# Kernel tuning notes

Hardware: AMD Instinct MI355X
Metric: run time of the kernel (lower is better)

Reference implementation:

```python
import jax, jax.numpy as jnp
import numpy as np

B, CN, DEG, IN_F, OUT_F, K = 32, 1024, 2, 128, 128, 10
NODES = [1, 16, 128, 1024]


def setup_inputs() -> dict:
    key = jax.random.key(0)
    ks = jax.random.split(key, 16)
    d = {}
    for i, n in enumerate(NODES):
        d[f"tree{i}"] = jax.random.normal(ks[i], (B, n, IN_F), dtype=jnp.float32)
    for i in range(4):
        d[f"Uw{i}"] = jax.random.normal(ks[4 + i], (IN_F, OUT_F), dtype=jnp.float32) * 0.05
        d[f"Ub{i}"] = jnp.zeros((OUT_F,), dtype=jnp.float32)
    d["W_up"] = jax.random.normal(ks[8], (CN, IN_F, DEG * IN_F), dtype=jnp.float32) * 0.05
    d["Fw0"] = jax.random.normal(ks[9], (IN_F, K * IN_F), dtype=jnp.float32) * 0.05
    d["Fb0"] = jnp.zeros((K * IN_F,), dtype=jnp.float32)
    d["Fw1"] = jax.random.normal(ks[10], (K * IN_F, OUT_F), dtype=jnp.float32) * 0.05
    d["Fb1"] = jnp.zeros((OUT_F,), dtype=jnp.float32)
    d["b_bias"] = jax.random.normal(ks[11], (1, DEG * CN, OUT_F), dtype=jnp.float32) * 0.05
    return d


def reference(tree0, tree1, tree2, tree3,
              Uw0, Ub0, Uw1, Ub1, Uw2, Ub2, Uw3, Ub3,
              W_up, Fw0, Fb0, Fw1, Fb1, b_bias):
    tree = [tree0, tree1, tree2, tree3]
    Uw = [Uw0, Uw1, Uw2, Uw3]
    Ub = [Ub0, Ub1, Ub2, Ub3]
    curr_node = W_up.shape[0]
    in_feat = W_up.shape[1]
    degree = W_up.shape[2] // in_feat

    # Ancestor info: project each depth, then tile each ancestor node's
    # projected vector to cover its descendants at the current level.
    anc = jnp.zeros((tree[0].shape[0], curr_node, Uw0.shape[1]), dtype=tree0.dtype)
    for t, w, b in zip(tree, Uw, Ub):
        Q = t @ w + b                       # [B, anc_node, out_feat]
        rep = curr_node // t.shape[1]
        anc = anc + jnp.repeat(Q, rep, axis=1)  # == tf.tile([1,1,rep]) + reshape

    # Per-node unique-weight upsample: [B,n,1,in] @ [n,in,deg*in]
    nl = jnp.einsum('bni,nio->bno', tree[-1], W_up)            # [B, CN, deg*in]
    nl = nl.reshape(nl.shape[0], curr_node * degree, in_feat)   # [B, CN*deg, in]
    nl = (nl @ Fw0 + Fb0) @ Fw1 + Fb1                           # Dense chain
    nl = nl + jnp.repeat(anc, degree, axis=1)                   # broadcast ancestors
    nl = nl + b_bias
    return jnp.where(nl >= 0, nl, 0.2 * nl)                     # LeakyReLU(0.2)
```

## Files before the change

kernel.cpp:

```cpp
#include <hip/hip_runtime.h>
#include <stdint.h>


using short8   = __attribute__((ext_vector_type(8))) short;
using floatx16 = __attribute__((ext_vector_type(16))) float;

__device__ __forceinline__ unsigned short f2bf(float f) {
    unsigned int u = __builtin_bit_cast(unsigned int, f);
    return (unsigned short)((u + 0x8000u) >> 16);
}

#define FB_OFF  524288
#define FF_OFF  524416
#define UW_OFF  532608

__global__ __launch_bounds__(256) void ffused_p1(
    const float* __restrict__ Fw0, const float* __restrict__ Fb0,
    const float* __restrict__ Fw1, float* __restrict__ P)
{
    const int kc = blockIdx.x;
    const int i  = blockIdx.y;
    const int j  = threadIdx.x & 127;
    const int il = threadIdx.x >> 7;
    const int k0 = kc * 160 + il * 80;
    const float* __restrict__ src = (i < 128) ? (Fw0 + (size_t)i * 1280) : Fb0;
    float acc = 0.f;
    #pragma unroll 8
    for (int kk = 0; kk < 80; ++kk)
        acc += src[k0 + kk] * Fw1[(size_t)(k0 + kk) * 128 + j];
    P[(size_t)(kc * 2 + il) * 16512 + i * 128 + j] = acc;
}

__global__ __launch_bounds__(256) void prep2(
    const float* __restrict__ P, const float* __restrict__ Fb1,
    const float* __restrict__ Uw0, const float* __restrict__ Uw1,
    const float* __restrict__ Uw2, const float* __restrict__ Uw3,
    unsigned short* __restrict__ FfusedBF, float* __restrict__ Fbias,
    unsigned short* __restrict__ UwBF)
{
    if (blockIdx.x < 65) {
        const int idx = blockIdx.x * 256 + threadIdx.x;
        if (idx >= 16512) return;
        const int i = idx >> 7, j = idx & 127;
        float s = 0.f;
        #pragma unroll
        for (int p = 0; p < 16; ++p) s += P[(size_t)p * 16512 + idx];
        if (i < 128) FfusedBF[(((i >> 3) * 128) + j) * 8 + (i & 7)] = f2bf(s);
        else         Fbias[j] = s + Fb1[j];
    } else {
        const int bx  = blockIdx.x - 65;
        const int mat = bx >> 4;
        const int kg  = bx & 15;
        const float* __restrict__ Uw = (mat == 0) ? Uw0 : (mat == 1) ? Uw1
                                     : (mat == 2) ? Uw2 : Uw3;
        const int col = threadIdx.x & 127;
        const int kh  = threadIdx.x >> 7;
        #pragma unroll
        for (int q = 0; q < 4; ++q) {
            const int kk = kh * 4 + q;
            const float v = Uw[(size_t)(kg * 8 + kk) * 128 + col];
            UwBF[(((size_t)(mat * 16 + kg) * 128) + col) * 8 + kk] = f2bf(v);
        }
    }
}

__global__ __launch_bounds__(256, 2) void tree_main(
    const float* __restrict__ t0, const float* __restrict__ t1,
    const float* __restrict__ t2, const float* __restrict__ t3,
    const float* __restrict__ Ub0, const float* __restrict__ Ub1,
    const float* __restrict__ Ub2, const float* __restrict__ Ub3,
    const float* __restrict__ Wup, const float* __restrict__ bbias,
    const unsigned short* __restrict__ FfusedBF,
    const unsigned short* __restrict__ UwBF,
    const float* __restrict__ Fbias,
    float* __restrict__ out)
{
    const int n    = blockIdx.x;
    const int tid  = threadIdx.x;
    const int w    = tid >> 6;
    const int lane = tid & 63;
    const int l31  = lane & 31;
    const int half = lane >> 5;
    const int colq = w * 32 + l31;
    const int i2   = n >> 3;

    __shared__ __align__(16) unsigned char smem_raw[64 * 33 * 8 * 2];
    unsigned short* Alds = (unsigned short*)smem_raw;
    unsigned short* Ulds = (unsigned short*)smem_raw;

    const float* __restrict__ Wbase =
        Wup + (size_t)n * 32768 + (half * 8) * 256 + w * 64 + l31;
    float Wa0[8], Wa1[8], Wb0[8], Wb1[8], Wc0[8], Wc1[8], Wd0[8], Wd1[8];
#define LOADW(P0, P1, WT) \
    { const float* __restrict__ wp = Wbase + (WT) * 16 * 256; \
      _Pragma("unroll") \
      for (int jj = 0; jj < 8; ++jj) { P0[jj] = wp[jj * 256]; P1[jj] = wp[32 + jj * 256]; } }
    LOADW(Wa0, Wa1, 0) LOADW(Wb0, Wb1, 1) LOADW(Wc0, Wc1, 2) LOADW(Wd0, Wd1, 3)

    #pragma unroll
    for (int mi = 0; mi < 4; ++mi) {
        const float* __restrict__ base = (mi == 0) ? t0 : (mi == 1) ? t1
                                       : (mi == 2) ? t2 : t3;
        #pragma unroll
        for (int i = 0; i < 4; ++i) {
            const int idx = i * 256 + tid;
            const int b   = idx >> 5;
            const int q   = idx & 31;
            int row;
            if      (mi == 0) row = b;
            else if (mi == 1) row = b * 16 + (i2 >> 3);
            else if (mi == 2) row = b * 128 + i2;
            else              row = b * 1024 + n;
            const float4 v = *reinterpret_cast<const float4*>(
                base + (size_t)row * 128 + q * 4);
            ushort4 u;
            u.x = f2bf(v.x); u.y = f2bf(v.y); u.z = f2bf(v.z); u.w = f2bf(v.w);
            *reinterpret_cast<ushort4*>(
                &Alds[((mi * 16 + (q >> 1)) * 33 + b) * 8 + (q & 1) * 4]) = u;
        }
    }
    __syncthreads();

    floatx16 qacc, accT0, accT1;
    #pragma unroll
    for (int r = 0; r < 16; ++r) { qacc[r] = 0.f; accT0[r] = 0.f; accT1[r] = 0.f; }

    #pragma unroll
    for (int ks = 0; ks < 24; ++ks) {
        const int kg = 2 * ks + half;
        const short8 a  = *reinterpret_cast<const short8*>(&Alds[(kg * 33 + l31) * 8]);
        const short8 bf = *reinterpret_cast<const short8*>(
            &UwBF[((size_t)kg * 128 + colq) * 8]);
        qacc = __builtin_amdgcn_mfma_f32_32x32x16_bf16(a, bf, qacc, 0, 0, 0);
    }

#define WBODY(P0, P1, WT) \
    { const int kg = 48 + 2 * (WT) + half; \
      const short8 a  = *reinterpret_cast<const short8*>(&Alds[(kg * 33 + l31) * 8]); \
      const short8 bf = *reinterpret_cast<const short8*>( \
          &UwBF[((size_t)kg * 128 + colq) * 8]); \
      qacc = __builtin_amdgcn_mfma_f32_32x32x16_bf16(a, bf, qacc, 0, 0, 0); \
      short8 a0, a1; \
      _Pragma("unroll") \
      for (int jj = 0; jj < 8; ++jj) { \
          a0[jj] = (short)f2bf(P0[jj]); a1[jj] = (short)f2bf(P1[jj]); } \
      accT0 = __builtin_amdgcn_mfma_f32_32x32x16_bf16(a0, a, accT0, 0, 0, 0); \
      accT1 = __builtin_amdgcn_mfma_f32_32x32x16_bf16(a1, a, accT1, 0, 0, 0); }

    WBODY(Wa0, Wa1, 0) LOADW(Wa0, Wa1, 4)
    WBODY(Wb0, Wb1, 1) LOADW(Wb0, Wb1, 5)
    WBODY(Wc0, Wc1, 2) LOADW(Wc0, Wc1, 6)
    WBODY(Wd0, Wd1, 3) LOADW(Wd0, Wd1, 7)
    WBODY(Wa0, Wa1, 4)
    WBODY(Wb0, Wb1, 5)
    WBODY(Wc0, Wc1, 6)
    WBODY(Wd0, Wd1, 7)

    __syncthreads();

    #pragma unroll
    for (int tt = 0; tt < 2; ++tt) {
        const floatx16 Av = tt ? accT1 : accT0;
        #pragma unroll
        for (int r = 0; r < 16; ++r) {
            const int cm = w * 64 + tt * 32 + ((r & 3) + 8 * (r >> 2) + 4 * half);
            const int d  = cm >> 7;
            const int cp = cm & 127;
            Ulds[(((cp >> 3) * 65) + d * 32 + l31) * 8 + (cp & 7)] = f2bf(Av[r]);
        }
    }
    __syncthreads();

    const float ubsum = Ub0[colq] + Ub1[colq] + Ub2[colq] + Ub3[colq] + Fbias[colq];
    const float bb0 = bbias[(size_t)(2 * n + 0) * 128 + colq];
    const float bb1 = bbias[(size_t)(2 * n + 1) * 128 + colq];

    floatx16 o0, o1;
    #pragma unroll
    for (int r = 0; r < 16; ++r) { o0[r] = 0.f; o1[r] = 0.f; }
    #pragma unroll
    for (int ks = 0; ks < 8; ++ks) {
        const int kg2 = 2 * ks + half;
        const short8 a0 = *reinterpret_cast<const short8*>(&Ulds[(kg2 * 65 + l31) * 8]);
        const short8 a1 = *reinterpret_cast<const short8*>(&Ulds[(kg2 * 65 + 32 + l31) * 8]);
        const short8 bf = *reinterpret_cast<const short8*>(
            &FfusedBF[(((size_t)kg2 * 128) + colq) * 8]);
        o0 = __builtin_amdgcn_mfma_f32_32x32x16_bf16(a0, bf, o0, 0, 0, 0);
        o1 = __builtin_amdgcn_mfma_f32_32x32x16_bf16(a1, bf, o1, 0, 0, 0);
    }

    #pragma unroll
    for (int r = 0; r < 16; ++r) {
        const int brow = (r & 3) + 8 * (r >> 2) + 4 * half;
        const float addc = qacc[r] + ubsum;
        float v0 = o0[r] + addc + bb0;
        float v1 = o1[r] + addc + bb1;
        v0 = (v0 >= 0.f) ? v0 : 0.2f * v0;
        v1 = (v1 >= 0.f) ? v1 : 0.2f * v1;
        const size_t idx0 = ((size_t)brow * 2048 + 2 * n) * 128 + colq;
        out[idx0]       = v0;
        out[idx0 + 128] = v1;
    }
}

extern "C" void kernel_launch(void* const* d_in, const int* in_sizes, int n_in,
                              void* d_out, int out_size, void* d_ws, size_t ws_size,
                              hipStream_t stream) {
    const float* t0  = (const float*)d_in[0];
    const float* t1  = (const float*)d_in[1];
    const float* t2  = (const float*)d_in[2];
    const float* t3  = (const float*)d_in[3];
    const float* Uw0 = (const float*)d_in[4];
    const float* Ub0 = (const float*)d_in[5];
    const float* Uw1 = (const float*)d_in[6];
    const float* Ub1 = (const float*)d_in[7];
    const float* Uw2 = (const float*)d_in[8];
    const float* Ub2 = (const float*)d_in[9];
    const float* Uw3 = (const float*)d_in[10];
    const float* Ub3 = (const float*)d_in[11];
    const float* Wup = (const float*)d_in[12];
    const float* Fw0 = (const float*)d_in[13];
    const float* Fb0 = (const float*)d_in[14];
    const float* Fw1 = (const float*)d_in[15];
    const float* Fb1 = (const float*)d_in[16];
    const float* bb  = (const float*)d_in[17];

    float* ws = (float*)d_ws;
    float* P              = ws;
    float* Fbias          = ws + FB_OFF;
    unsigned short* FfBF  = (unsigned short*)(ws + FF_OFF);
    unsigned short* UwBF  = (unsigned short*)(ws + UW_OFF);

    ffused_p1<<<dim3(8, 129), 256, 0, stream>>>(Fw0, Fb0, Fw1, P);
    prep2<<<129, 256, 0, stream>>>(P, Fb1, Uw0, Uw1, Uw2, Uw3, FfBF, Fbias, UwBF);
    tree_main<<<1024, 256, 0, stream>>>(t0, t1, t2, t3,
                                        Ub0, Ub1, Ub2, Ub3,
                                        Wup, bb, FfBF, UwBF,
                                        Fbias, (float*)d_out);
}
```

Before: 264.7 us.

## Stream W_up tiles through double-buffered LDS via async global_load_lds

```diff
diff --git a/kernel.cpp b/kernel.cpp
--- a/kernel.cpp
+++ b/kernel.cpp
@@ -84,18 +84,26 @@
     const int colq = w * 32 + l31;
     const int i2   = n >> 3;
 
-    __shared__ __align__(16) unsigned char smem_raw[64 * 33 * 8 * 2];
+    __shared__ __align__(16) unsigned char smem_raw[33792 + 2 * 16384];
     unsigned short* Alds = (unsigned short*)smem_raw;
     unsigned short* Ulds = (unsigned short*)smem_raw;
-
-    const float* __restrict__ Wbase =
-        Wup + (size_t)n * 32768 + (half * 8) * 256 + w * 64 + l31;
-    float Wa0[8], Wa1[8], Wb0[8], Wb1[8], Wc0[8], Wc1[8], Wd0[8], Wd1[8];
-#define LOADW(P0, P1, WT) \
-    { const float* __restrict__ wp = Wbase + (WT) * 16 * 256; \
-      _Pragma("unroll") \
-      for (int jj = 0; jj < 8; ++jj) { P0[jj] = wp[jj * 256]; P1[jj] = wp[32 + jj * 256]; } }
-    LOADW(Wa0, Wa1, 0) LOADW(Wb0, Wb1, 1) LOADW(Wc0, Wc1, 2) LOADW(Wd0, Wd1, 3)
+    float* wbuf0 = (float*)(smem_raw + 33792);
+    float* wbuf1 = (float*)(smem_raw + 33792 + 16384);
+
+    const float* __restrict__ Wtile = Wup + (size_t)n * 32768;
+#define ISSUE_W(T, WB) \
+    { _Pragma("unroll") \
+      for (int q = 0; q < 4; ++q) { \
+        const int chunk = (tid >> 6) * 4 + q; \
+        const float* gp = Wtile + (T) * 4096 + chunk * 256 + (tid & 63) * 4; \
+        float* lp = (WB) + chunk * 256; \
+        __builtin_amdgcn_global_load_lds( \
+            (const __attribute__((address_space(1))) unsigned int*)gp, \
+            (__attribute__((address_space(3))) unsigned int*)lp, 16, 0, 0); \
+      } }
+
+    ISSUE_W(0, wbuf0)
+    ISSUE_W(1, wbuf1)
 
     #pragma unroll
     for (int mi = 0; mi < 4; ++mi) {
@@ -134,7 +142,7 @@
         qacc = __builtin_amdgcn_mfma_f32_32x32x16_bf16(a, bf, qacc, 0, 0, 0);
     }
 
-#define WBODY(P0, P1, WT) \
+#define WBODY_L(WT, WB) \
     { const int kg = 48 + 2 * (WT) + half; \
       const short8 a  = *reinterpret_cast<const short8*>(&Alds[(kg * 33 + l31) * 8]); \
       const short8 bf = *reinterpret_cast<const short8*>( \
@@ -143,18 +151,19 @@
       short8 a0, a1; \
       _Pragma("unroll") \
       for (int jj = 0; jj < 8; ++jj) { \
-          a0[jj] = (short)f2bf(P0[jj]); a1[jj] = (short)f2bf(P1[jj]); } \
+          a0[jj] = (short)f2bf((WB)[(half * 8 + jj) * 256 + w * 64 + l31]); \
+          a1[jj] = (short)f2bf((WB)[(half * 8 + jj) * 256 + w * 64 + 32 + l31]); } \
       accT0 = __builtin_amdgcn_mfma_f32_32x32x16_bf16(a0, a, accT0, 0, 0, 0); \
       accT1 = __builtin_amdgcn_mfma_f32_32x32x16_bf16(a1, a, accT1, 0, 0, 0); }
 
-    WBODY(Wa0, Wa1, 0) LOADW(Wa0, Wa1, 4)
-    WBODY(Wb0, Wb1, 1) LOADW(Wb0, Wb1, 5)
-    WBODY(Wc0, Wc1, 2) LOADW(Wc0, Wc1, 6)
-    WBODY(Wd0, Wd1, 3) LOADW(Wd0, Wd1, 7)
-    WBODY(Wa0, Wa1, 4)
-    WBODY(Wb0, Wb1, 5)
-    WBODY(Wc0, Wc1, 6)
-    WBODY(Wd0, Wd1, 7)
+    WBODY_L(0, wbuf0) __syncthreads(); ISSUE_W(2, wbuf0)
+    WBODY_L(1, wbuf1) __syncthreads(); ISSUE_W(3, wbuf1)
+    WBODY_L(2, wbuf0) __syncthreads(); ISSUE_W(4, wbuf0)
+    WBODY_L(3, wbuf1) __syncthreads(); ISSUE_W(5, wbuf1)
+    WBODY_L(4, wbuf0) __syncthreads(); ISSUE_W(6, wbuf0)
+    WBODY_L(5, wbuf1) __syncthreads(); ISSUE_W(7, wbuf1)
+    WBODY_L(6, wbuf0) __syncthreads();
+    WBODY_L(7, wbuf1)
 
     __syncthreads();
 
```

Result: no change. 263.8 us (-0.3%).
